# Kernel optimization log

Measured on AMD Instinct MI355X. Metric: run time of the kernel, lower is better.

Reference implementation:

```python
import jax, jax.numpy as jnp
import numpy as np

B, N, C = 8, 4096, 512
H = 8
HD = C // H  # 64
SCALE = HD ** -0.5


def setup_inputs() -> dict:
    key = jax.random.key(0)
    ks = jax.random.split(key, 6)
    x = jax.random.normal(ks[0], (B, N, C), dtype=jnp.float32)
    # nn.Linear(dim, dim*3, bias=False): weight [3C, C]
    w_qkv = jax.random.normal(ks[1], (3 * C, C), dtype=jnp.float32) * (C ** -0.5)
    # nn.Linear(dim, dim): weight [C, C], bias [C]
    w_proj = jax.random.normal(ks[2], (C, C), dtype=jnp.float32) * (C ** -0.5)
    b_proj = jnp.zeros((C,), dtype=jnp.float32)
    w_q = jax.random.normal(ks[3], (H, HD), dtype=jnp.float32)
    w_k = jax.random.normal(ks[4], (H, HD), dtype=jnp.float32)
    return {"x": x, "w_qkv": w_qkv, "w_proj": w_proj, "b_proj": b_proj,
            "w_q": w_q, "w_k": w_k}


def reference(x, w_qkv, w_proj, b_proj, w_q, w_k):
    b, n, c = x.shape
    # qkv projection: [B,N,3C] -> (3, B, H, N, HD)
    qkv = jnp.einsum('bnc,dc->bnd', x, w_qkv)
    qkv = qkv.reshape(b, n, 3, H, HD).transpose(2, 0, 3, 1, 4)
    q, k, v = qkv[0], qkv[1], qkv[2]  # each [B,H,N,HD]

    # alpha attention pooling of q -> global query [B,H,HD]
    alpha = jax.nn.softmax(jnp.einsum('bhnc,hc->bhn', q, w_q) * SCALE, axis=-1)
    global_q = jnp.einsum('bhn,bhnc->bhc', alpha, q)

    # p = broadcast global_q over k; beta pooling of k -> global key
    p = global_q[:, :, None, :] * k  # [B,H,N,HD] (attn_drop is identity in eval)
    beta = jax.nn.softmax(jnp.einsum('bhnc,hc->bhn', p, w_k) * SCALE, axis=-1)
    global_k = jnp.einsum('bhn,bhnc->bhc', beta, k)

    # u = global_k broadcast * v, then merge heads
    u = global_k[:, :, None, :] * v  # [B,H,N,HD]
    u_flat = u.transpose(0, 2, 1, 3).reshape(b, n, c)
    q_flat = q.transpose(0, 2, 1, 3).reshape(b, n, c)

    out = jnp.einsum('bnc,dc->bnd', u_flat, w_proj) + b_proj + q_flat
    return out
```

## Files before the change

### kernel.cpp

```cpp
#include <hip/hip_runtime.h>
#include <hip/hip_bf16.h>
#include <math.h>

#define B_  8
#define N_  4096
#define C_  512
#define H_  8
#define HD_ 64
#define M_  (B_*N_)
#define K_  C_
#define D3_ (3*C_)
#define SCALE_ 0.125f

using f32x4  = __attribute__((ext_vector_type(4))) float;
using bf16x8 = __attribute__((ext_vector_type(8))) short;

__device__ __forceinline__ unsigned short f2bf(float f) {
    unsigned int u = __builtin_bit_cast(unsigned int, f);
    u += 0x7FFFu + ((u >> 16) & 1u);
    return (unsigned short)(u >> 16);
}
__device__ __forceinline__ float bf2f(unsigned short s) {
    unsigned int u = ((unsigned int)s) << 16;
    return __builtin_bit_cast(float, u);
}

__device__ __forceinline__ void gl_lds16(const void* g, void* l) {
    __builtin_amdgcn_global_load_lds(
        (const __attribute__((address_space(1))) unsigned int*)(g),
        (__attribute__((address_space(3))) unsigned int*)(l), 16, 0, 0);
}

__global__ __launch_bounds__(256, 2)
void k_gemm1(const unsigned short* __restrict__ Ag, const unsigned short* __restrict__ Bg,
             const float* __restrict__ Wq,
             float* __restrict__ outQ, unsigned short* __restrict__ outK,
             unsigned short* __restrict__ outV,
             float* __restrict__ pm1, float* __restrict__ ps1, float* __restrict__ pv1)
{
    __shared__ __align__(16) unsigned char lds[16384];
    const int m0 = blockIdx.x * 128;
    const int d0 = blockIdx.y * 128;
    const int t = threadIdx.x, lane = t & 63, w = t >> 6;
    const int wr = w >> 1, wc = w & 1;
    const int lrow = lane >> 2, lslot = lane & 3;
    const int fr = lane & 15, g = lane >> 4;

    f32x4 acc[4][4];
    #pragma unroll
    for (int i = 0; i < 4; ++i)
        #pragma unroll
        for (int j = 0; j < 4; ++j) acc[i][j] = (f32x4){0.f,0.f,0.f,0.f};

    for (int k0 = 0; k0 < K_; k0 += 32) {
        #pragma unroll
        for (int s = 0; s < 2; ++s) {
            const int seg = w*2 + s;
            const int row = seg*16 + lrow;
            const int ch  = lslot ^ ((row >> 1) & 3);
            gl_lds16(Ag + (size_t)(m0+row)*K_ + k0 + ch*8, lds + seg*1024);
            gl_lds16(Bg + (size_t)(d0+row)*K_ + k0 + ch*8, lds + 8192 + seg*1024);
        }
        __syncthreads();
        bf16x8 aF[4], bF[4];
        #pragma unroll
        for (int i = 0; i < 4; ++i) {
            const int r = wr*64 + i*16 + fr;
            const int sl = g ^ ((r >> 1) & 3);
            aF[i] = *(const bf16x8*)(lds + r*64 + sl*16);
        }
        #pragma unroll
        for (int j = 0; j < 4; ++j) {
            const int r = wc*64 + j*16 + fr;
            const int sl = g ^ ((r >> 1) & 3);
            bF[j] = *(const bf16x8*)(lds + 8192 + r*64 + sl*16);
        }
        #pragma unroll
        for (int i = 0; i < 4; ++i)
            #pragma unroll
            for (int j = 0; j < 4; ++j)
                acc[i][j] = __builtin_amdgcn_mfma_f32_16x16x32_bf16(aF[i], bF[j], acc[i][j], 0, 0, 0);
        __syncthreads();
    }

    #pragma unroll
    for (int i = 0; i < 4; ++i)
        #pragma unroll
        for (int j = 0; j < 4; ++j) {
            const int trow = wr*64 + i*16 + g*4;
            const int tcol = wc*64 + j*16 + fr;
            const int d = d0 + tcol;
            #pragma unroll
            for (int p = 0; p < 4; ++p) {
                const size_t m = (size_t)(m0 + trow + p);
                const float vv = acc[i][j][p];
                if (d0 < C_)          outQ[m*C_ + d] = vv;
                else if (d0 < 2*C_)   outK[m*C_ + (d - C_)] = f2bf(vv);
                else                  outV[m*C_ + (d - 2*C_)] = f2bf(vv);
            }
        }

    if (d0 < C_) {
        const int head = (d0 >> 6) + wc;
        const int b = m0 >> 12;
        const int bh = b*8 + head;
        const int mchunk = (m0 & 4095) >> 7;
        const int chunk = mchunk*8 + wr*4 + g;
        float wqv[4];
        #pragma unroll
        for (int j = 0; j < 4; ++j) wqv[j] = Wq[head*HD_ + j*16 + fr] * SCALE_;

        float s[4][4];
        #pragma unroll
        for (int i = 0; i < 4; ++i)
            #pragma unroll
            for (int p = 0; p < 4; ++p) {
                float d = acc[i][0][p]*wqv[0] + acc[i][1][p]*wqv[1]
                        + acc[i][2][p]*wqv[2] + acc[i][3][p]*wqv[3];
                d += __shfl_xor(d, 1); d += __shfl_xor(d, 2);
                d += __shfl_xor(d, 4); d += __shfl_xor(d, 8);
                s[i][p] = d;
            }
        float mx = s[0][0];
        #pragma unroll
        for (int i = 0; i < 4; ++i)
            #pragma unroll
            for (int p = 0; p < 4; ++p) mx = fmaxf(mx, s[i][p]);
        float e[4][4]; float ssum = 0.f;
        #pragma unroll
        for (int i = 0; i < 4; ++i)
            #pragma unroll
            for (int p = 0; p < 4; ++p) { e[i][p] = __expf(s[i][p] - mx); ssum += e[i][p]; }
        #pragma unroll
        for (int j = 0; j < 4; ++j) {
            float pvj = 0.f;
            #pragma unroll
            for (int i = 0; i < 4; ++i)
                #pragma unroll
                for (int p = 0; p < 4; ++p) pvj = fmaf(e[i][p], acc[i][j][p], pvj);
            pv1[((size_t)bh*256 + chunk)*64 + j*16 + fr] = pvj;
        }
        if (fr == 0) { pm1[bh*256 + chunk] = mx; ps1[bh*256 + chunk] = ssum; }
    }
}

__global__ __launch_bounds__(256)
void k_comb1(const float* __restrict__ pm, const float* __restrict__ ps,
             const float* __restrict__ pv, float* __restrict__ gq)
{
    __shared__ float red[4];
    __shared__ float sred[4];
    __shared__ float pvs[4][64];
    __shared__ float stat[2];
    const int bh = blockIdx.x;
    const int t = threadIdx.x, lane = t & 63, wv = t >> 6;

    float m = pm[bh*256 + t];
    #pragma unroll
    for (int off = 32; off; off >>= 1) m = fmaxf(m, __shfl_xor(m, off));
    if (lane == 0) red[wv] = m;
    __syncthreads();
    if (t == 0) stat[0] = fmaxf(fmaxf(red[0],red[1]), fmaxf(red[2],red[3]));
    __syncthreads();
    m = stat[0];

    float e  = __expf(pm[bh*256 + t] - m);
    float sp = ps[bh*256 + t] * e;
    #pragma unroll
    for (int off = 32; off; off >>= 1) sp += __shfl_xor(sp, off);
    if (lane == 0) sred[wv] = sp;
    __syncthreads();
    if (t == 0) stat[1] = sred[0]+sred[1]+sred[2]+sred[3];

    float acc = 0.f;
    for (int c0 = 0; c0 < 64; ++c0) {
        const int ch = wv*64 + c0;
        const float ec = __expf(pm[bh*256 + ch] - m);
        acc = fmaf(pv[((size_t)bh*256 + ch)*64 + lane], ec, acc);
    }
    pvs[wv][lane] = acc;
    __syncthreads();
    if (t < 64) gq[bh*64 + t] = (pvs[0][t]+pvs[1][t]+pvs[2][t]+pvs[3][t]) / stat[1];
}

__global__ __launch_bounds__(256)
void k_pool2(const unsigned short* __restrict__ kb, const float* __restrict__ w_k,
             const float* __restrict__ gq,
             float* __restrict__ pm2, float* __restrict__ ps2, float* __restrict__ pv2)
{
    __shared__ float mred[4];
    __shared__ float sl[4][64];
    __shared__ float sred2[4];
    const int bid = blockIdx.x;
    const int bh = bid >> 4, ch = bid & 15;
    const int b = bh >> 3, h = bh & 7;
    const int t = threadIdx.x, lane = t & 63, wv = t >> 6;
    const float wk = w_k[h*64 + lane] * gq[bh*64 + lane] * SCALE_;
    const unsigned short* base = kb + ((size_t)b*N_ + ch*256)*C_ + h*64 + lane;

    float mw = -1e30f, sw = 0.f, pvw = 0.f;
    for (int n0 = wv*4; n0 < 256; n0 += 16) {
        float x0 = bf2f(base[(size_t)(n0+0)*C_]);
        float x1 = bf2f(base[(size_t)(n0+1)*C_]);
        float x2 = bf2f(base[(size_t)(n0+2)*C_]);
        float x3 = bf2f(base[(size_t)(n0+3)*C_]);
        float s0 = x0*wk, s1 = x1*wk, s2 = x2*wk, s3 = x3*wk;
        #pragma unroll
        for (int off = 32; off; off >>= 1) {
            s0 += __shfl_xor(s0, off); s1 += __shfl_xor(s1, off);
            s2 += __shfl_xor(s2, off); s3 += __shfl_xor(s3, off);
        }
        const float mx = fmaxf(fmaxf(s0,s1), fmaxf(s2,s3));
        const float mn = fmaxf(mw, mx);
        const float f  = __expf(mw - mn);
        const float e0 = __expf(s0 - mn), e1 = __expf(s1 - mn);
        const float e2 = __expf(s2 - mn), e3 = __expf(s3 - mn);
        sw  = sw*f  + (e0+e1+e2+e3);
        pvw = pvw*f + e0*x0 + e1*x1 + e2*x2 + e3*x3;
        mw = mn;
    }
    if (lane == 0) mred[wv] = mw;
    __syncthreads();
    const float mb = fmaxf(fmaxf(mred[0],mred[1]), fmaxf(mred[2],mred[3]));
    const float f = __expf(mw - mb);
    sl[wv][lane] = pvw * f;
    if (lane == 0) sred2[wv] = sw * f;
    __syncthreads();
    if (t < 64) {
        pv2[(size_t)bid*64 + t] = sl[0][t]+sl[1][t]+sl[2][t]+sl[3][t];
        if (t == 0) ps2[bid] = sred2[0]+sred2[1]+sred2[2]+sred2[3];
        if (t == 1) pm2[bid] = mb;
    }
}

__global__ __launch_bounds__(256)
void k_fold(const float* __restrict__ wp, const float* __restrict__ pm2,
            const float* __restrict__ ps2, const float* __restrict__ pv2,
            unsigned short* __restrict__ wpb)
{
    const int i = blockIdx.x*256 + threadIdx.x;
    const int idx4 = i*4;
    const int b  = idx4 >> 18;
    const int wi = idx4 & 262143;
    const int k  = idx4 & 511;
    const int h  = k >> 6, hd = k & 63;
    const int bh = b*8 + h;

    float m = pm2[bh*16];
    #pragma unroll
    for (int c = 1; c < 16; ++c) m = fmaxf(m, pm2[bh*16 + c]);
    float s = 0.f, g0 = 0.f, g1 = 0.f, g2 = 0.f, g3 = 0.f;
    #pragma unroll
    for (int c = 0; c < 16; ++c) {
        const float e = __expf(pm2[bh*16 + c] - m);
        s = fmaf(ps2[bh*16 + c], e, s);
        const float4 pvv = *(const float4*)(pv2 + (size_t)(bh*16 + c)*64 + hd);
        g0 = fmaf(pvv.x, e, g0); g1 = fmaf(pvv.y, e, g1);
        g2 = fmaf(pvv.z, e, g2); g3 = fmaf(pvv.w, e, g3);
    }
    const float inv = 1.0f / s;
    const float4 wv4 = *(const float4*)(wp + wi);
    ushort4 r;
    r.x = f2bf(wv4.x * g0 * inv); r.y = f2bf(wv4.y * g1 * inv);
    r.z = f2bf(wv4.z * g2 * inv); r.w = f2bf(wv4.w * g3 * inv);
    ((ushort4*)wpb)[i] = r;
}

__global__ __launch_bounds__(256, 2)
void k_gemm2(const unsigned short* __restrict__ Ag, const unsigned short* __restrict__ Wpb,
             const float* __restrict__ bproj, float* __restrict__ out)
{
    __shared__ __align__(16) unsigned char lds[16384];
    const int m0 = blockIdx.x * 128;
    const int d0 = blockIdx.y * 128;
    const int b  = m0 >> 12;
    const unsigned short* Bg = Wpb + (size_t)b * C_ * C_;
    const int t = threadIdx.x, lane = t & 63, w = t >> 6;
    const int wr = w >> 1, wc = w & 1;
    const int lrow = lane >> 2, lslot = lane & 3;
    const int fr = lane & 15, g = lane >> 4;

    f32x4 acc[4][4];
    #pragma unroll
    for (int i = 0; i < 4; ++i)
        #pragma unroll
        for (int j = 0; j < 4; ++j) acc[i][j] = (f32x4){0.f,0.f,0.f,0.f};

    for (int k0 = 0; k0 < K_; k0 += 32) {
        #pragma unroll
        for (int s = 0; s < 2; ++s) {
            const int seg = w*2 + s;
            const int row = seg*16 + lrow;
            const int ch  = lslot ^ ((row >> 1) & 3);
            gl_lds16(Ag + (size_t)(m0+row)*K_ + k0 + ch*8, lds + seg*1024);
            gl_lds16(Bg + (size_t)(d0+row)*K_ + k0 + ch*8, lds + 8192 + seg*1024);
        }
        __syncthreads();
        bf16x8 aF[4], bF[4];
        #pragma unroll
        for (int i = 0; i < 4; ++i) {
            const int r = wr*64 + i*16 + fr;
            const int sl = g ^ ((r >> 1) & 3);
            aF[i] = *(const bf16x8*)(lds + r*64 + sl*16);
        }
        #pragma unroll
        for (int j = 0; j < 4; ++j) {
            const int r = wc*64 + j*16 + fr;
            const int sl = g ^ ((r >> 1) & 3);
            bF[j] = *(const bf16x8*)(lds + 8192 + r*64 + sl*16);
        }
        #pragma unroll
        for (int i = 0; i < 4; ++i)
            #pragma unroll
            for (int j = 0; j < 4; ++j)
                acc[i][j] = __builtin_amdgcn_mfma_f32_16x16x32_bf16(aF[i], bF[j], acc[i][j], 0, 0, 0);
        __syncthreads();
    }

    #pragma unroll
    for (int i = 0; i < 4; ++i)
        #pragma unroll
        for (int j = 0; j < 4; ++j) {
            const int trow = wr*64 + i*16 + g*4;
            const int tcol = wc*64 + j*16 + fr;
            const int d = d0 + tcol;
            const float bp = bproj[d];
            #pragma unroll
            for (int p = 0; p < 4; ++p) {
                const size_t off = (size_t)(m0 + trow + p)*C_ + d;
                out[off] = acc[i][j][p] + bp + out[off];
            }
        }
}

__global__ void k_cvt2(const float* __restrict__ a, const float* __restrict__ bsrc,
                       unsigned short* __restrict__ oa, unsigned short* __restrict__ ob,
                       int na4, int nb4)
{
    int i = blockIdx.x*256 + threadIdx.x;
    const int stride = gridDim.x*256;
    const int tot = na4 + nb4;
    for (; i < tot; i += stride) {
        if (i < na4) {
            const float4 f = ((const float4*)a)[i];
            ushort4 r; r.x = f2bf(f.x); r.y = f2bf(f.y); r.z = f2bf(f.z); r.w = f2bf(f.w);
            ((ushort4*)oa)[i] = r;
        } else {
            const int j = i - na4;
            const float4 f = ((const float4*)bsrc)[j];
            ushort4 r; r.x = f2bf(f.x); r.y = f2bf(f.y); r.z = f2bf(f.z); r.w = f2bf(f.w);
            ((ushort4*)ob)[j] = r;
        }
    }
}

extern "C" void kernel_launch(void* const* d_in, const int* in_sizes, int n_in,
                              void* d_out, int out_size, void* d_ws, size_t ws_size,
                              hipStream_t stream)
{
    (void)in_sizes; (void)n_in; (void)out_size; (void)ws_size;
    const float* x      = (const float*)d_in[0];
    const float* w_qkv  = (const float*)d_in[1];
    const float* w_proj = (const float*)d_in[2];
    const float* b_proj = (const float*)d_in[3];
    const float* w_q    = (const float*)d_in[4];
    const float* w_k    = (const float*)d_in[5];
    float* out = (float*)d_out;

    unsigned short* xb  = (unsigned short*)d_ws;
    unsigned short* wqb = xb  + (size_t)M_*K_;
    unsigned short* kb  = wqb + (size_t)D3_*K_;
    unsigned short* vb  = kb  + (size_t)M_*C_;
    unsigned short* wpb = vb  + (size_t)M_*C_;
    float* gq  = (float*)(wpb + (size_t)8*C_*C_);
    float* pm1 = gq  + 64*64;
    float* ps1 = pm1 + 64*256;
    float* pv1 = ps1 + 64*256;
    float* pm2 = pv1 + (size_t)64*256*64;
    float* ps2 = pm2 + 1024;
    float* pv2 = ps2 + 1024;

    k_cvt2<<<2048, 256, 0, stream>>>(x, w_qkv, xb, wqb, M_*K_/4, D3_*K_/4);

    dim3 g1(M_/128, D3_/128);
    k_gemm1<<<g1, 256, 0, stream>>>(xb, wqb, w_q, out, kb, vb, pm1, ps1, pv1);

    k_comb1<<<64, 256, 0, stream>>>(pm1, ps1, pv1, gq);
    k_pool2<<<1024, 256, 0, stream>>>(kb, w_k, gq, pm2, ps2, pv2);
    k_fold<<<2048, 256, 0, stream>>>(w_proj, pm2, ps2, pv2, wpb);

    dim3 g2(M_/128, C_/128);
    k_gemm2<<<g2, 256, 0, stream>>>(vb, wpb, b_proj, out);
}
```

Measured before the change: 271.0 us.

## Fuse global-query combine into pool2 and remap GEMM tiles across XCDs

Removes the k_comb1 launch; each k_pool2 block now recomputes the global query for its (batch, head) directly from the per-chunk max, sum and weighted-value partials. Both GEMMs switch to a 1D grid with a block-index remap that groups the tiles handled by each of the 8 XCDs so they share input rows in cache. The fused combine is redundantly repeated in 16 blocks per head, and each block walks 256 partial vectors serially before pooling.

```diff
diff --git a/kernel.cpp b/kernel.cpp
--- a/kernel.cpp
+++ b/kernel.cpp
@@ -39,8 +39,10 @@
              float* __restrict__ pm1, float* __restrict__ ps1, float* __restrict__ pv1)
 {
     __shared__ __align__(16) unsigned char lds[16384];
-    const int m0 = blockIdx.x * 128;
-    const int d0 = blockIdx.y * 128;
+    const int flat = blockIdx.x;
+    const int wgid = (flat & 7) * 384 + (flat >> 3);
+    const int m0 = (wgid / 12) * 128;
+    const int d0 = (wgid % 12) * 128;
     const int t = threadIdx.x, lane = t & 63, w = t >> 6;
     const int wr = w >> 1, wc = w & 1;
     const int lrow = lane >> 2, lslot = lane & 3;
@@ -145,47 +147,9 @@
 }
 
 __global__ __launch_bounds__(256)
-void k_comb1(const float* __restrict__ pm, const float* __restrict__ ps,
-             const float* __restrict__ pv, float* __restrict__ gq)
-{
-    __shared__ float red[4];
-    __shared__ float sred[4];
-    __shared__ float pvs[4][64];
-    __shared__ float stat[2];
-    const int bh = blockIdx.x;
-    const int t = threadIdx.x, lane = t & 63, wv = t >> 6;
-
-    float m = pm[bh*256 + t];
-    #pragma unroll
-    for (int off = 32; off; off >>= 1) m = fmaxf(m, __shfl_xor(m, off));
-    if (lane == 0) red[wv] = m;
-    __syncthreads();
-    if (t == 0) stat[0] = fmaxf(fmaxf(red[0],red[1]), fmaxf(red[2],red[3]));
-    __syncthreads();
-    m = stat[0];
-
-    float e  = __expf(pm[bh*256 + t] - m);
-    float sp = ps[bh*256 + t] * e;
-    #pragma unroll
-    for (int off = 32; off; off >>= 1) sp += __shfl_xor(sp, off);
-    if (lane == 0) sred[wv] = sp;
-    __syncthreads();
-    if (t == 0) stat[1] = sred[0]+sred[1]+sred[2]+sred[3];
-
-    float acc = 0.f;
-    for (int c0 = 0; c0 < 64; ++c0) {
-        const int ch = wv*64 + c0;
-        const float ec = __expf(pm[bh*256 + ch] - m);
-        acc = fmaf(pv[((size_t)bh*256 + ch)*64 + lane], ec, acc);
-    }
-    pvs[wv][lane] = acc;
-    __syncthreads();
-    if (t < 64) gq[bh*64 + t] = (pvs[0][t]+pvs[1][t]+pvs[2][t]+pvs[3][t]) / stat[1];
-}
-
-__global__ __launch_bounds__(256)
 void k_pool2(const unsigned short* __restrict__ kb, const float* __restrict__ w_k,
-             const float* __restrict__ gq,
+             const float* __restrict__ pm1, const float* __restrict__ ps1,
+             const float* __restrict__ pv1,
              float* __restrict__ pm2, float* __restrict__ ps2, float* __restrict__ pv2)
 {
     __shared__ float mred[4];
@@ -195,7 +159,21 @@
     const int bh = bid >> 4, ch = bid & 15;
     const int b = bh >> 3, h = bh & 7;
     const int t = threadIdx.x, lane = t & 63, wv = t >> 6;
-    const float wk = w_k[h*64 + lane] * gq[bh*64 + lane] * SCALE_;
+
+    float am = -1e30f;
+    for (int c = 0; c < 256; c += 4) {
+        const float4 p4 = *(const float4*)(pm1 + bh*256 + c);
+        am = fmaxf(am, fmaxf(fmaxf(p4.x, p4.y), fmaxf(p4.z, p4.w)));
+    }
+    float as = 0.f, gqv = 0.f;
+    for (int c = 0; c < 256; ++c) {
+        const float e = __expf(pm1[bh*256 + c] - am);
+        as  = fmaf(ps1[bh*256 + c], e, as);
+        gqv = fmaf(pv1[((size_t)bh*256 + c)*64 + lane], e, gqv);
+    }
+    gqv /= as;
+
+    const float wk = w_k[h*64 + lane] * gqv * SCALE_;
     const unsigned short* base = kb + ((size_t)b*N_ + ch*256)*C_ + h*64 + lane;
 
     float mw = -1e30f, sw = 0.f, pvw = 0.f;
@@ -271,8 +249,10 @@
              const float* __restrict__ bproj, float* __restrict__ out)
 {
     __shared__ __align__(16) unsigned char lds[16384];
-    const int m0 = blockIdx.x * 128;
-    const int d0 = blockIdx.y * 128;
+    const int flat = blockIdx.x;
+    const int wgid = (flat & 7) * 128 + (flat >> 3);
+    const int m0 = (wgid >> 2) * 128;
+    const int d0 = (wgid & 3) * 128;
     const int b  = m0 >> 12;
     const unsigned short* Bg = Wpb + (size_t)b * C_ * C_;
     const int t = threadIdx.x, lane = t & 63, w = t >> 6;
@@ -372,8 +352,7 @@
     unsigned short* kb  = wqb + (size_t)D3_*K_;
     unsigned short* vb  = kb  + (size_t)M_*C_;
     unsigned short* wpb = vb  + (size_t)M_*C_;
-    float* gq  = (float*)(wpb + (size_t)8*C_*C_);
-    float* pm1 = gq  + 64*64;
+    float* pm1 = (float*)(wpb + (size_t)8*C_*C_);
     float* ps1 = pm1 + 64*256;
     float* pv1 = ps1 + 64*256;
     float* pm2 = pv1 + (size_t)64*256*64;
@@ -382,13 +361,10 @@
 
     k_cvt2<<<2048, 256, 0, stream>>>(x, w_qkv, xb, wqb, M_*K_/4, D3_*K_/4);
 
-    dim3 g1(M_/128, D3_/128);
-    k_gemm1<<<g1, 256, 0, stream>>>(xb, wqb, w_q, out, kb, vb, pm1, ps1, pv1);
-
-    k_comb1<<<64, 256, 0, stream>>>(pm1, ps1, pv1, gq);
-    k_pool2<<<1024, 256, 0, stream>>>(kb, w_k, gq, pm2, ps2, pv2);
+    k_gemm1<<<3072, 256, 0, stream>>>(xb, wqb, w_q, out, kb, vb, pm1, ps1, pv1);
+
+    k_pool2<<<1024, 256, 0, stream>>>(kb, w_k, pm1, ps1, pv1, pm2, ps2, pv2);
     k_fold<<<2048, 256, 0, stream>>>(w_proj, pm2, ps2, pv2, wpb);
 
-    dim3 g2(M_/128, C_/128);
-    k_gemm2<<<g2, 256, 0, stream>>>(vb, wpb, b_proj, out);
-}
+    k_gemm2<<<1024, 256, 0, stream>>>(vb, wpb, b_proj, out);
+}
```

Result: no change. 274.9 us (+1.4%).
